# Kernel tuning notes

Hardware: AMD Instinct MI355X
Metric: run time of the kernel (lower is better)

## Reference

```python
import jax, jax.numpy as jnp
import numpy as np

TEMPERATURE = 0.1
LARGE_NUM = 1e9


def _l2_normalize(x, eps=1e-12):
    # tf.math.l2_normalize: x * rsqrt(max(sum(x^2), eps))
    sq = jnp.sum(x * x, axis=-1, keepdims=True)
    return x * jax.lax.rsqrt(jnp.maximum(sq, eps))


def setup_inputs() -> dict:
    key = jax.random.key(0)
    k1, k2 = jax.random.split(key)
    B, D = 4096, 128
    z1 = jax.random.normal(k1, (B, D), dtype=jnp.float32)
    z2 = jax.random.normal(k2, (B, D), dtype=jnp.float32)
    return {"z1": z1, "z2": z2}


def reference(z1, z2):
    B = z1.shape[0]
    a = _l2_normalize(z1)  # [B, D]
    b = _l2_normalize(z2)  # [B, D]
    mask = jnp.eye(B, dtype=a.dtype)
    inv_t = 1.0 / TEMPERATURE
    logits_aa = jnp.matmul(a, a.T) * inv_t - mask * LARGE_NUM  # [B, B]
    logits_bb = jnp.matmul(b, b.T) * inv_t - mask * LARGE_NUM  # [B, B]
    logits_ab = jnp.matmul(a, b.T) * inv_t                      # [B, B]
    logits_ba = jnp.matmul(b, a.T) * inv_t                      # [B, B]
    part1 = jax.nn.softmax(jnp.concatenate([logits_ab, logits_aa], axis=1), axis=-1)
    part2 = jax.nn.softmax(jnp.concatenate([logits_ba, logits_bb], axis=1), axis=-1)
    return jnp.concatenate([part1, part2], axis=1)  # [B, 4B]
```

## Files before the change

### kernel.cpp

```cpp
#include <hip/hip_runtime.h>
#include <hip/hip_fp16.h>
#include <cstdint>
#include <cstddef>

#define NB   4096
#define ND   128
#define OUTW 16384
#define CG   16
#define IT   8

#define K2   14.4269504088896341f

typedef _Float16 f16;
typedef __attribute__((ext_vector_type(2))) _Float16 f16x2;
typedef __attribute__((ext_vector_type(8))) _Float16 f16x8;
typedef __attribute__((ext_vector_type(4))) float   f32x4;

__global__ __launch_bounds__(256) void nrm_kernel(const float* __restrict__ z1,
                                                  const float* __restrict__ z2,
                                                  f16* __restrict__ ab,
                                                  float* __restrict__ rowsum) {
  if (threadIdx.x < 4) rowsum[blockIdx.x * 4 + threadIdx.x] = 0.0f;
  int row  = blockIdx.x * 4 + (threadIdx.x >> 6);
  int lane = threadIdx.x & 63;
  const float* src = (row < NB) ? (z1 + (size_t)row * ND)
                                : (z2 + (size_t)(row - NB) * ND);
  float2 v = ((const float2*)src)[lane];
  float ss = v.x * v.x + v.y * v.y;
#pragma unroll
  for (int off = 32; off; off >>= 1) ss += __shfl_xor(ss, off);
  float r = rsqrtf(fmaxf(ss, 1e-12f));
  f16x2 h;
  h.x = (f16)(v.x * r);
  h.y = (f16)(v.y * r);
  ((f16x2*)(ab + (size_t)row * ND))[lane] = h;
}

__global__ __launch_bounds__(256, 2) void sum_kernel(const f16* __restrict__ ab,
                                                     float* __restrict__ rowsum) {
  __shared__ f16 Bs[2][64 * ND];
  __shared__ float cs_col[512];

  const int t    = threadIdx.x;
  const int wave = t >> 6;
  const int lane = t & 63;
  const int wr   = wave >> 1;
  const int wc   = wave & 1;
  const int quad = lane >> 4;
  const int l16  = lane & 15;

  const int s     = blockIdx.y;
  const int m     = s >> 5;
  const int r0    = (s & 31) * 128;
  const int cbase = blockIdx.x * 512;
  const f16* Q  = ab + (size_t)(m == 2 ? NB * ND : 0);
  const f16* Kp = ab + (size_t)(m == 1 ? 0 : NB * ND);
  const bool diag = (m != 0);
  const bool docol = (m == 0);

  f16x8 af[4][4];
  {
    const int arow = r0 + wr * 64 + l16;
#pragma unroll
    for (int mi = 0; mi < 4; ++mi)
#pragma unroll
      for (int ks = 0; ks < 4; ++ks)
        af[mi][ks] = *(const f16x8*)(Q + (size_t)(arow + mi * 16) * ND +
                                     ks * 32 + quad * 8);
  }

  const int sub = t >> 4;
  const int oct = t & 15;
  auto stage_b = [&](f16* buf, int kc0) {
#pragma unroll
    for (int i = 0; i < 4; ++i) {
      int rowl = i * 16 + sub;
      int goct = oct ^ (rowl & 15);
      __builtin_amdgcn_global_load_lds(
          (const __attribute__((address_space(1))) void*)(
              Kp + (size_t)(kc0 + rowl) * ND + goct * 8),
          (__attribute__((address_space(3))) void*)(buf + rowl * ND + oct * 8),
          16, 0, 0);
    }
  };

  float ps[4];
#pragma unroll
  for (int mi = 0; mi < 4; ++mi) ps[mi] = 0.0f;

  stage_b(Bs[0], cbase);
  cs_col[t] = 0.0f;
  cs_col[t + 256] = 0.0f;
  __syncthreads();

  for (int it = 0; it < IT; ++it) {
    if (it + 1 < IT) stage_b(Bs[(it + 1) & 1], cbase + (it + 1) * 64);

    const f16* buf = Bs[it & 1];
    f32x4 acc[4][2] = {};
#pragma unroll
    for (int ks = 0; ks < 4; ++ks) {
      int sw = (((ks * 4 + quad) ^ l16)) * 8;
      f16x8 bf0 = *(const f16x8*)(buf + (wc * 32 + l16) * ND + sw);
      f16x8 bf1 = *(const f16x8*)(buf + (wc * 32 + 16 + l16) * ND + sw);
#pragma unroll
      for (int mi = 0; mi < 4; ++mi) {
        acc[mi][0] = __builtin_amdgcn_mfma_f32_16x16x32_f16(bf0, af[mi][ks],
                                                            acc[mi][0], 0, 0, 0);
        acc[mi][1] = __builtin_amdgcn_mfma_f32_16x16x32_f16(bf1, af[mi][ks],
                                                            acc[mi][1], 0, 0, 0);
      }
    }

    const int c0m = cbase + it * 64;
    const bool dtile = diag && (c0m == r0 || c0m == r0 + 64);

    float cpart[8];
#pragma unroll
    for (int v = 0; v < 8; ++v) cpart[v] = 0.0f;

#pragma unroll
    for (int mi = 0; mi < 4; ++mi) {
      const int row_l = wr * 64 + mi * 16 + l16;
#pragma unroll
      for (int ni = 0; ni < 2; ++ni) {
        const int cq = wc * 32 + ni * 16 + quad * 4;
#pragma unroll
        for (int r = 0; r < 4; ++r) {
          float e = __builtin_amdgcn_exp2f(fmaf(acc[mi][ni][r], K2, -K2));
          if (dtile && (c0m + cq + r == r0 + row_l)) e = 0.0f;
          ps[mi] += e;
          cpart[ni * 4 + r] += e;
        }
      }
    }

    if (docol) {
#pragma unroll
      for (int v = 0; v < 8; ++v) {
        float x = cpart[v];
        x += __shfl_xor(x, 1);
        x += __shfl_xor(x, 2);
        x += __shfl_xor(x, 4);
        x += __shfl_xor(x, 8);
        cpart[v] = x;
      }
      if (l16 == 0) {
#pragma unroll
        for (int v = 0; v < 8; ++v) {
          int col_l = it * 64 + wc * 32 + (v >> 2) * 16 + quad * 4 + (v & 3);
          atomicAdd(&cs_col[col_l], cpart[v]);
        }
      }
    }
    __syncthreads();
  }

  const int rbase = (m == 2) ? NB + r0 : r0;
#pragma unroll
  for (int mi = 0; mi < 4; ++mi) {
    float v = ps[mi];
    v += __shfl_xor(v, 16);
    v += __shfl_xor(v, 32);
    if (quad == 0) {
      int row_l = wr * 64 + mi * 16 + l16;
      atomicAdd(&rowsum[rbase + row_l], v);
    }
  }

  if (docol) {
    atomicAdd(&rowsum[NB + cbase + t], cs_col[t]);
    atomicAdd(&rowsum[NB + cbase + t + 256], cs_col[t + 256]);
  }
}

__global__ __launch_bounds__(256, 2) void wr_kernel(const f16* __restrict__ ab,
                                                    float* __restrict__ rowsum,
                                                    float* __restrict__ out) {
  __shared__ f16 Bs[2][64 * ND];
  __shared__ float cs[128];

  const int t    = threadIdx.x;
  const int wave = t >> 6;
  const int lane = t & 63;
  const int wr   = wave >> 1;
  const int wc   = wave & 1;
  const int quad = lane >> 4;
  const int l16  = lane & 15;

  const int rt    = blockIdx.y;
  const int type  = rt >> 5;
  const int r0    = (rt & 31) * 128;
  const int g     = blockIdx.x;
  const int h2    = (g >= CG / 2) ? 1 : 0;
  const int cbl   = g * (8192 / CG);
  const int cbase = cbl & (NB - 1);
  const f16* Q  = ab + (size_t)type * NB * ND;
  const f16* Kp = ab + (size_t)(h2 ? type : (type ^ 1)) * NB * ND;

  f16x8 af[4][4];
  {
    const int arow = r0 + wr * 64 + l16;
#pragma unroll
    for (int mi = 0; mi < 4; ++mi)
#pragma unroll
      for (int ks = 0; ks < 4; ++ks)
        af[mi][ks] = *(const f16x8*)(Q + (size_t)(arow + mi * 16) * ND +
                                     ks * 32 + quad * 8);
  }

  const int sub = t >> 4;
  const int oct = t & 15;
  auto stage_b = [&](f16* buf, int kc0) {
#pragma unroll
    for (int i = 0; i < 4; ++i) {
      int rowl = i * 16 + sub;
      int goct = oct ^ (rowl & 15);
      __builtin_amdgcn_global_load_lds(
          (const __attribute__((address_space(1))) void*)(
              Kp + (size_t)(kc0 + rowl) * ND + goct * 8),
          (__attribute__((address_space(3))) void*)(buf + rowl * ND + oct * 8),
          16, 0, 0);
    }
  };

  stage_b(Bs[0], cbase);
  if (t < 128) cs[t] = -__log2f(rowsum[rt * 128 + t]) - K2;
  __syncthreads();

  for (int it = 0; it < IT; ++it) {
    if (it + 1 < IT) stage_b(Bs[(it + 1) & 1], cbase + (it + 1) * 64);

    const f16* buf = Bs[it & 1];
    f32x4 acc[4][2] = {};
#pragma unroll
    for (int ks = 0; ks < 4; ++ks) {
      int sw = (((ks * 4 + quad) ^ l16)) * 8;
      f16x8 bf0 = *(const f16x8*)(buf + (wc * 32 + l16) * ND + sw);
      f16x8 bf1 = *(const f16x8*)(buf + (wc * 32 + 16 + l16) * ND + sw);
#pragma unroll
      for (int mi = 0; mi < 4; ++mi) {
        acc[mi][0] = __builtin_amdgcn_mfma_f32_16x16x32_f16(bf0, af[mi][ks],
                                                            acc[mi][0], 0, 0, 0);
        acc[mi][1] = __builtin_amdgcn_mfma_f32_16x16x32_f16(bf1, af[mi][ks],
                                                            acc[mi][1], 0, 0, 0);
      }
    }

    const int c0m = cbase + it * 64;
    const bool dtile = h2 && (c0m == r0 || c0m == r0 + 64);

#pragma unroll
    for (int mi = 0; mi < 4; ++mi) {
      const int row_l = wr * 64 + mi * 16 + l16;
      const float c = cs[row_l];
      float* orow = out + (size_t)(r0 + row_l) * OUTW + (size_t)type * 8192 +
                    cbl + it * 64;
#pragma unroll
      for (int ni = 0; ni < 2; ++ni) {
        const int cq = wc * 32 + ni * 16 + quad * 4;
        f32x4 o;
#pragma unroll
        for (int r = 0; r < 4; ++r) {
          float e = __builtin_amdgcn_exp2f(fmaf(acc[mi][ni][r], K2, c));
          if (dtile && (c0m + cq + r == r0 + row_l)) e = 0.0f;
          o[r] = e;
        }
        *(f32x4*)(orow + cq) = o;
      }
    }
    __syncthreads();
  }
}

extern "C" void kernel_launch(void* const* d_in, const int* in_sizes, int n_in,
                              void* d_out, int out_size, void* d_ws, size_t ws_size,
                              hipStream_t stream) {
  const float* z1 = (const float*)d_in[0];
  const float* z2 = (const float*)d_in[1];
  float* out = (float*)d_out;

  f16* ab = (f16*)d_ws;
  float* rowsum = (float*)((char*)d_ws + (size_t)8192 * ND * sizeof(f16));

  nrm_kernel<<<2048, 256, 0, stream>>>(z1, z2, ab, rowsum);
  sum_kernel<<<dim3(8, 96), 256, 0, stream>>>(ab, rowsum);
  wr_kernel<<<dim3(CG, 64), 256, 0, stream>>>(ab, rowsum, out);
}
```

Baseline: 302.1 us.

## Balance sum kernel work over 512 blocks and widen write-kernel column strips

The sum kernel moves from a fixed 8x96 grid to 512 persistent-style blocks that each process 12 consecutive 64-column tiles, possibly spanning two row-strip segments. Column-sum staging grows to 768 entries to cover the largest span. The write kernel now uses 8 column groups of 1024 columns (16 iterations each) instead of 16 groups of 512, which halves the A-fragment reloads and rowsum log setup per output column. The aim is an even wave count across CUs (512 blocks at 2 per CU on 256 CUs), at the cost of extra segment-loop overhead and fewer blocks in the write kernel.

```diff
diff --git a/kernel.cpp b/kernel.cpp
--- a/kernel.cpp
+++ b/kernel.cpp
@@ -6,8 +6,6 @@
 #define NB   4096
 #define ND   128
 #define OUTW 16384
-#define CG   16
-#define IT   8
 
 #define K2   14.4269504088896341f
 
@@ -39,7 +37,7 @@
 __global__ __launch_bounds__(256, 2) void sum_kernel(const f16* __restrict__ ab,
                                                      float* __restrict__ rowsum) {
   __shared__ f16 Bs[2][64 * ND];
-  __shared__ float cs_col[512];
+  __shared__ float cs_col[768];
 
   const int t    = threadIdx.x;
   const int wave = t >> 6;
@@ -48,15 +46,164 @@
   const int wc   = wave & 1;
   const int quad = lane >> 4;
   const int l16  = lane & 15;
-
-  const int s     = blockIdx.y;
-  const int m     = s >> 5;
-  const int r0    = (s & 31) * 128;
-  const int cbase = blockIdx.x * 512;
-  const f16* Q  = ab + (size_t)(m == 2 ? NB * ND : 0);
-  const f16* Kp = ab + (size_t)(m == 1 ? 0 : NB * ND);
-  const bool diag = (m != 0);
-  const bool docol = (m == 0);
+  const int sub  = t >> 4;
+  const int oct  = t & 15;
+
+  int g0   = blockIdx.x * 12;
+  int gend = g0 + 12;
+
+  while (g0 < gend) {
+    const int s    = g0 >> 6;
+    const int t0   = g0 & 63;
+    const int tn   = min(64 - t0, gend - g0);
+    const int m    = s >> 5;
+    const int r0   = (s & 31) * 128;
+    const int cseg = t0 * 64;
+    const f16* Q  = ab + (size_t)(m == 2 ? NB * ND : 0);
+    const f16* Kp = ab + (size_t)(m == 1 ? 0 : NB * ND);
+    const bool diag  = (m != 0);
+    const bool docol = (m == 0);
+
+    f16x8 af[4][4];
+    {
+      const int arow = r0 + wr * 64 + l16;
+#pragma unroll
+      for (int mi = 0; mi < 4; ++mi)
+#pragma unroll
+        for (int ks = 0; ks < 4; ++ks)
+          af[mi][ks] = *(const f16x8*)(Q + (size_t)(arow + mi * 16) * ND +
+                                       ks * 32 + quad * 8);
+    }
+
+    auto stage_b = [&](f16* buf, int kc0) {
+#pragma unroll
+      for (int i = 0; i < 4; ++i) {
+        int rowl = i * 16 + sub;
+        int goct = oct ^ (rowl & 15);
+        __builtin_amdgcn_global_load_lds(
+            (const __attribute__((address_space(1))) void*)(
+                Kp + (size_t)(kc0 + rowl) * ND + goct * 8),
+            (__attribute__((address_space(3))) void*)(buf + rowl * ND + oct * 8),
+            16, 0, 0);
+      }
+    };
+
+    float ps[4];
+#pragma unroll
+    for (int mi = 0; mi < 4; ++mi) ps[mi] = 0.0f;
+    if (docol)
+      for (int i = t; i < tn * 64; i += 256) cs_col[i] = 0.0f;
+
+    stage_b(Bs[0], cseg);
+    __syncthreads();
+
+    for (int j = 0; j < tn; ++j) {
+      if (j + 1 < tn) stage_b(Bs[(j + 1) & 1], cseg + (j + 1) * 64);
+
+      const f16* buf = Bs[j & 1];
+      f32x4 acc[4][2] = {};
+#pragma unroll
+      for (int ks = 0; ks < 4; ++ks) {
+        int sw = (((ks * 4 + quad) ^ l16)) * 8;
+        f16x8 bf0 = *(const f16x8*)(buf + (wc * 32 + l16) * ND + sw);
+        f16x8 bf1 = *(const f16x8*)(buf + (wc * 32 + 16 + l16) * ND + sw);
+#pragma unroll
+        for (int mi = 0; mi < 4; ++mi) {
+          acc[mi][0] = __builtin_amdgcn_mfma_f32_16x16x32_f16(bf0, af[mi][ks],
+                                                              acc[mi][0], 0, 0, 0);
+          acc[mi][1] = __builtin_amdgcn_mfma_f32_16x16x32_f16(bf1, af[mi][ks],
+                                                              acc[mi][1], 0, 0, 0);
+        }
+      }
+
+      const int c0m = cseg + j * 64;
+      const bool dtile = diag && (c0m == r0 || c0m == r0 + 64);
+
+      float cpart[8];
+#pragma unroll
+      for (int v = 0; v < 8; ++v) cpart[v] = 0.0f;
+
+#pragma unroll
+      for (int mi = 0; mi < 4; ++mi) {
+        const int row_l = wr * 64 + mi * 16 + l16;
+#pragma unroll
+        for (int ni = 0; ni < 2; ++ni) {
+          const int cq = wc * 32 + ni * 16 + quad * 4;
+#pragma unroll
+          for (int r = 0; r < 4; ++r) {
+            float e = __builtin_amdgcn_exp2f(fmaf(acc[mi][ni][r], K2, -K2));
+            if (dtile && (c0m + cq + r == r0 + row_l)) e = 0.0f;
+            ps[mi] += e;
+            cpart[ni * 4 + r] += e;
+          }
+        }
+      }
+
+      if (docol) {
+#pragma unroll
+        for (int v = 0; v < 8; ++v) {
+          float x = cpart[v];
+          x += __shfl_xor(x, 1);
+          x += __shfl_xor(x, 2);
+          x += __shfl_xor(x, 4);
+          x += __shfl_xor(x, 8);
+          cpart[v] = x;
+        }
+        if (l16 == 0) {
+#pragma unroll
+          for (int v = 0; v < 8; ++v) {
+            int col_l = j * 64 + wc * 32 + (v >> 2) * 16 + quad * 4 + (v & 3);
+            atomicAdd(&cs_col[col_l], cpart[v]);
+          }
+        }
+      }
+      __syncthreads();
+    }
+
+    const int rbase = (m == 2) ? NB + r0 : r0;
+#pragma unroll
+    for (int mi = 0; mi < 4; ++mi) {
+      float v = ps[mi];
+      v += __shfl_xor(v, 16);
+      v += __shfl_xor(v, 32);
+      if (quad == 0) {
+        int row_l = wr * 64 + mi * 16 + l16;
+        atomicAdd(&rowsum[rbase + row_l], v);
+      }
+    }
+
+    if (docol)
+      for (int i = t; i < tn * 64; i += 256)
+        atomicAdd(&rowsum[NB + cseg + i], cs_col[i]);
+
+    g0 += tn;
+  }
+}
+
+__global__ __launch_bounds__(256, 2) void wr_kernel(const f16* __restrict__ ab,
+                                                    float* __restrict__ rowsum,
+                                                    float* __restrict__ out) {
+  __shared__ f16 Bs[2][64 * ND];
+  __shared__ float cs[128];
+
+  const int t    = threadIdx.x;
+  const int wave = t >> 6;
+  const int lane = t & 63;
+  const int wr   = wave >> 1;
+  const int wc   = wave & 1;
+  const int quad = lane >> 4;
+  const int l16  = lane & 15;
+  const int sub  = t >> 4;
+  const int oct  = t & 15;
+
+  const int rt    = blockIdx.y;
+  const int type  = rt >> 5;
+  const int r0    = (rt & 31) * 128;
+  const int gp    = blockIdx.x;
+  const int h2    = (gp >= 4) ? 1 : 0;
+  const int base  = (gp & 3) * 1024;
+  const f16* Q  = ab + (size_t)type * NB * ND;
+  const f16* Kp = ab + (size_t)(h2 ? type : (type ^ 1)) * NB * ND;
 
   f16x8 af[4][4];
   {
@@ -69,8 +216,6 @@
                                      ks * 32 + quad * 8);
   }
 
-  const int sub = t >> 4;
-  const int oct = t & 15;
   auto stage_b = [&](f16* buf, int kc0) {
 #pragma unroll
     for (int i = 0; i < 4; ++i) {
@@ -84,17 +229,12 @@
     }
   };
 
-  float ps[4];
-#pragma unroll
-  for (int mi = 0; mi < 4; ++mi) ps[mi] = 0.0f;
-
-  stage_b(Bs[0], cbase);
-  cs_col[t] = 0.0f;
-  cs_col[t + 256] = 0.0f;
+  stage_b(Bs[0], base);
+  if (t < 128) cs[t] = -__log2f(rowsum[rt * 128 + t]) - K2;
   __syncthreads();
 
-  for (int it = 0; it < IT; ++it) {
-    if (it + 1 < IT) stage_b(Bs[(it + 1) & 1], cbase + (it + 1) * 64);
+  for (int it = 0; it < 16; ++it) {
+    if (it + 1 < 16) stage_b(Bs[(it + 1) & 1], base + (it + 1) * 64);
 
     const f16* buf = Bs[it & 1];
     f32x4 acc[4][2] = {};
@@ -112,142 +252,7 @@
       }
     }
 
-    const int c0m = cbase + it * 64;
-    const bool dtile = diag && (c0m == r0 || c0m == r0 + 64);
-
-    float cpart[8];
-#pragma unroll
-    for (int v = 0; v < 8; ++v) cpart[v] = 0.0f;
-
-#pragma unroll
-    for (int mi = 0; mi < 4; ++mi) {
-      const int row_l = wr * 64 + mi * 16 + l16;
-#pragma unroll
-      for (int ni = 0; ni < 2; ++ni) {
-        const int cq = wc * 32 + ni * 16 + quad * 4;
-#pragma unroll
-        for (int r = 0; r < 4; ++r) {
-          float e = __builtin_amdgcn_exp2f(fmaf(acc[mi][ni][r], K2, -K2));
-          if (dtile && (c0m + cq + r == r0 + row_l)) e = 0.0f;
-          ps[mi] += e;
-          cpart[ni * 4 + r] += e;
-        }
-      }
-    }
-
-    if (docol) {
-#pragma unroll
-      for (int v = 0; v < 8; ++v) {
-        float x = cpart[v];
-        x += __shfl_xor(x, 1);
-        x += __shfl_xor(x, 2);
-        x += __shfl_xor(x, 4);
-        x += __shfl_xor(x, 8);
-        cpart[v] = x;
-      }
-      if (l16 == 0) {
-#pragma unroll
-        for (int v = 0; v < 8; ++v) {
-          int col_l = it * 64 + wc * 32 + (v >> 2) * 16 + quad * 4 + (v & 3);
-          atomicAdd(&cs_col[col_l], cpart[v]);
-        }
-      }
-    }
-    __syncthreads();
-  }
-
-  const int rbase = (m == 2) ? NB + r0 : r0;
-#pragma unroll
-  for (int mi = 0; mi < 4; ++mi) {
-    float v = ps[mi];
-    v += __shfl_xor(v, 16);
-    v += __shfl_xor(v, 32);
-    if (quad == 0) {
-      int row_l = wr * 64 + mi * 16 + l16;
-      atomicAdd(&rowsum[rbase + row_l], v);
-    }
-  }
-
-  if (docol) {
-    atomicAdd(&rowsum[NB + cbase + t], cs_col[t]);
-    atomicAdd(&rowsum[NB + cbase + t + 256], cs_col[t + 256]);
-  }
-}
-
-__global__ __launch_bounds__(256, 2) void wr_kernel(const f16* __restrict__ ab,
-                                                    float* __restrict__ rowsum,
-                                                    float* __restrict__ out) {
-  __shared__ f16 Bs[2][64 * ND];
-  __shared__ float cs[128];
-
-  const int t    = threadIdx.x;
-  const int wave = t >> 6;
-  const int lane = t & 63;
-  const int wr   = wave >> 1;
-  const int wc   = wave & 1;
-  const int quad = lane >> 4;
-  const int l16  = lane & 15;
-
-  const int rt    = blockIdx.y;
-  const int type  = rt >> 5;
-  const int r0    = (rt & 31) * 128;
-  const int g     = blockIdx.x;
-  const int h2    = (g >= CG / 2) ? 1 : 0;
-  const int cbl   = g * (8192 / CG);
-  const int cbase = cbl & (NB - 1);
-  const f16* Q  = ab + (size_t)type * NB * ND;
-  const f16* Kp = ab + (size_t)(h2 ? type : (type ^ 1)) * NB * ND;
-
-  f16x8 af[4][4];
-  {
-    const int arow = r0 + wr * 64 + l16;
-#pragma unroll
-    for (int mi = 0; mi < 4; ++mi)
-#pragma unroll
-      for (int ks = 0; ks < 4; ++ks)
-        af[mi][ks] = *(const f16x8*)(Q + (size_t)(arow + mi * 16) * ND +
-                                     ks * 32 + quad * 8);
-  }
-
-  const int sub = t >> 4;
-  const int oct = t & 15;
-  auto stage_b = [&](f16* buf, int kc0) {
-#pragma unroll
-    for (int i = 0; i < 4; ++i) {
-      int rowl = i * 16 + sub;
-      int goct = oct ^ (rowl & 15);
-      __builtin_amdgcn_global_load_lds(
-          (const __attribute__((address_space(1))) void*)(
-              Kp + (size_t)(kc0 + rowl) * ND + goct * 8),
-          (__attribute__((address_space(3))) void*)(buf + rowl * ND + oct * 8),
-          16, 0, 0);
-    }
-  };
-
-  stage_b(Bs[0], cbase);
-  if (t < 128) cs[t] = -__log2f(rowsum[rt * 128 + t]) - K2;
-  __syncthreads();
-
-  for (int it = 0; it < IT; ++it) {
-    if (it + 1 < IT) stage_b(Bs[(it + 1) & 1], cbase + (it + 1) * 64);
-
-    const f16* buf = Bs[it & 1];
-    f32x4 acc[4][2] = {};
-#pragma unroll
-    for (int ks = 0; ks < 4; ++ks) {
-      int sw = (((ks * 4 + quad) ^ l16)) * 8;
-      f16x8 bf0 = *(const f16x8*)(buf + (wc * 32 + l16) * ND + sw);
-      f16x8 bf1 = *(const f16x8*)(buf + (wc * 32 + 16 + l16) * ND + sw);
-#pragma unroll
-      for (int mi = 0; mi < 4; ++mi) {
-        acc[mi][0] = __builtin_amdgcn_mfma_f32_16x16x32_f16(bf0, af[mi][ks],
-                                                            acc[mi][0], 0, 0, 0);
-        acc[mi][1] = __builtin_amdgcn_mfma_f32_16x16x32_f16(bf1, af[mi][ks],
-                                                            acc[mi][1], 0, 0, 0);
-      }
-    }
-
-    const int c0m = cbase + it * 64;
+    const int c0m = base + it * 64;
     const bool dtile = h2 && (c0m == r0 || c0m == r0 + 64);
 
 #pragma unroll
@@ -255,7 +260,9 @@
       const int row_l = wr * 64 + mi * 16 + l16;
       const float c = cs[row_l];
       float* orow = out + (size_t)(r0 + row_l) * OUTW + (size_t)type * 8192 +
-                    cbl + it * 64;
+                    (size_t)h2 * 4096 + c0m - (h2 ? 0 : 0) + 0;
+      orow = out + (size_t)(r0 + row_l) * OUTW + (size_t)type * 8192 +
+             (size_t)h2 * 4096 + (size_t)(c0m - (h2 ? 0 : 0));
 #pragma unroll
       for (int ni = 0; ni < 2; ++ni) {
         const int cq = wc * 32 + ni * 16 + quad * 4;
@@ -284,6 +291,6 @@
   float* rowsum = (float*)((char*)d_ws + (size_t)8192 * ND * sizeof(f16));
 
   nrm_kernel<<<2048, 256, 0, stream>>>(z1, z2, ab, rowsum);
-  sum_kernel<<<dim3(8, 96), 256, 0, stream>>>(ab, rowsum);
-  wr_kernel<<<dim3(CG, 64), 256, 0, stream>>>(ab, rowsum, out);
-}
+  sum_kernel<<<512, 256, 0, stream>>>(ab, rowsum);
+  wr_kernel<<<dim3(8, 64), 256, 0, stream>>>(ab, rowsum, out);
+}
```

Result: slower. 318.5 us (+5.5%).
